# Kernel optimization log

Hardware: AMD Instinct MI355X
Metric: run time of the kernel (lower is better)

## Reference

```python
import jax, jax.numpy as jnp
import numpy as np
from jax import lax


def _gaussian_1d(size=5, std=1.0):
    x = np.arange(size) - (size - 1) / 2.0
    return np.exp(-0.5 * (x / std) ** 2).astype(np.float32)  # scipy.signal.gaussian (unnormalized)


def _conv(x, w):
    # x: (N,1,H,W), w: (O,1,kh,kw), stride 1, SAME padding (matches torch padding=k//2)
    return lax.conv_general_dilated(x, w, (1, 1), 'SAME',
                                    dimension_numbers=('NCHW', 'OIHW', 'NCHW'))


def setup_inputs() -> dict:
    key = jax.random.key(0)
    img = jax.random.normal(key, (8, 1, 1024, 1024), dtype=jnp.float32)

    g = _gaussian_1d(5, 1.0)
    gauss_h = jnp.asarray(g.reshape(1, 1, 1, 5))
    gauss_v = jnp.asarray(g.reshape(1, 1, 5, 1))

    sob = np.array([[1, 0, -1], [2, 0, -2], [1, 0, -1]], dtype=np.float32)
    sobel_h = jnp.asarray(sob.reshape(1, 1, 3, 3))
    sobel_v = jnp.asarray(sob.T.reshape(1, 1, 3, 3))

    f0 = np.array([[0, 0, 0], [0, 1, -1], [0, 0, 0]], dtype=np.float32)
    f45 = np.array([[0, 0, 0], [0, 1, 0], [0, 0, -1]], dtype=np.float32)
    f90 = np.array([[0, 0, 0], [0, 1, 0], [0, -1, 0]], dtype=np.float32)
    f135 = np.array([[0, 0, 0], [0, 1, 0], [-1, 0, 0]], dtype=np.float32)
    f180 = np.array([[0, 0, 0], [-1, 1, 0], [0, 0, 0]], dtype=np.float32)
    f225 = np.array([[-1, 0, 0], [0, 1, 0], [0, 0, 0]], dtype=np.float32)
    f270 = np.array([[0, -1, 0], [0, 1, 0], [0, 0, 0]], dtype=np.float32)
    f315 = np.array([[0, 0, -1], [0, 1, 0], [0, 0, 0]], dtype=np.float32)
    dir_w = jnp.asarray(np.stack([f0, f45, f90, f135, f180, f225, f270, f315])[:, None])  # (8,1,3,3)

    return {"img": img, "gauss_h": gauss_h, "gauss_v": gauss_v,
            "sobel_h": sobel_h, "sobel_v": sobel_v, "dir_w": dir_w}


def reference(img, gauss_h, gauss_v, sobel_h, sobel_v, dir_w):
    THRESHOLD = 2.0
    # separable gaussian blur
    blurred = _conv(_conv(img, gauss_h), gauss_v)  # (N,1,H,W)
    # sobel gradients
    grad_x = _conv(blurred, sobel_h)
    grad_y = _conv(blurred, sobel_v)
    grad_mag = jnp.sqrt(grad_x ** 2 + grad_y ** 2)  # (N,1,H,W)
    # orientation quantized to multiples of 45 deg in [0, 360]
    grad_orientation = jnp.arctan2(grad_y, grad_x) * (180.0 / 3.14159) + 180.0
    grad_orientation = jnp.round(grad_orientation / 45.0) * 45.0
    # directional NMS (vectorized replacement of the batch-looped gather)
    all_filtered = _conv(grad_mag, dir_w)  # (N,8,H,W)
    idx_pos = (jnp.round(grad_orientation / 45.0).astype(jnp.int32)) % 8  # (N,1,H,W)
    idx_neg = (idx_pos + 4) % 8
    sel_pos = jnp.take_along_axis(all_filtered, idx_pos, axis=1)  # (N,1,H,W)
    sel_neg = jnp.take_along_axis(all_filtered, idx_neg, axis=1)
    is_max = jnp.minimum(sel_pos, sel_neg) > 0.0
    thin_edges = jnp.where(is_max, grad_mag, 0.0)
    thresholded = jnp.where(thin_edges < THRESHOLD, 0.0, thin_edges)  # computed but unused, as in source
    del thresholded
    early_threshold = jnp.where(grad_mag < THRESHOLD, 0.0, grad_mag)
    return early_threshold
```

## Files before the change

### kernel.cpp

```cpp
#include <hip/hip_runtime.h>
#include <math.h>


#define TW 64
#define TH 32
#define HALO 3
#define SW (TW + 2 * HALO)
#define SH (TH + 2 * HALO)
#define H_IMG 1024
#define W_IMG 1024

__global__ __launch_bounds__(256) void canny_fused(
    const float* __restrict__ img,
    const float* __restrict__ gauss,
    float* __restrict__ out)
{
    __shared__ float s_img[SH][SW];
    __shared__ float s_t[SH][SW];
    __shared__ float s_b[SH][SW];

    const int tx0 = blockIdx.x * TW;
    const int ty0 = blockIdx.y * TH;
    const int b   = blockIdx.z;
    const int tid = threadIdx.x;

    const float g0 = gauss[0];
    const float g1 = gauss[1];
    const float g2 = gauss[2];

    const float* imgb = img + (size_t)b * (H_IMG * W_IMG);

    for (int i = tid; i < SH * SW; i += 256) {
        int sr = i / SW, sc = i - sr * SW;
        int gy = ty0 + sr - HALO;
        int gx = tx0 + sc - HALO;
        float v = 0.0f;
        if (gy >= 0 && gy < H_IMG && gx >= 0 && gx < W_IMG)
            v = imgb[gy * W_IMG + gx];
        s_img[sr][sc] = v;
    }
    __syncthreads();

    for (int i = tid; i < SH * SW; i += 256) {
        int sr = i / SW, sc = i - sr * SW;
        if (sc >= 2 && sc <= SW - 3) {
            s_t[sr][sc] = g0 * (s_img[sr][sc - 2] + s_img[sr][sc + 2])
                        + g1 * (s_img[sr][sc - 1] + s_img[sr][sc + 1])
                        + g2 *  s_img[sr][sc];
        }
    }
    __syncthreads();

    for (int i = tid; i < SH * SW; i += 256) {
        int sr = i / SW, sc = i - sr * SW;
        if (sr >= 2 && sr <= SH - 3 && sc >= 2 && sc <= SW - 3) {
            int gy = ty0 + sr - HALO;
            int gx = tx0 + sc - HALO;
            float v = 0.0f;
            if (gy >= 0 && gy < H_IMG && gx >= 0 && gx < W_IMG) {
                v = g0 * (s_t[sr - 2][sc] + s_t[sr + 2][sc])
                  + g1 * (s_t[sr - 1][sc] + s_t[sr + 1][sc])
                  + g2 *  s_t[sr][sc];
            }
            s_b[sr][sc] = v;
        }
    }
    __syncthreads();

    float* outb = out + (size_t)b * (H_IMG * W_IMG);
    for (int j = tid; j < TH * TW; j += 256) {
        int ly = j / TW, lx = j - ly * TW;
        int sr = ly + HALO, sc = lx + HALO;
        float tl = s_b[sr - 1][sc - 1], tm = s_b[sr - 1][sc], tr = s_b[sr - 1][sc + 1];
        float ml = s_b[sr    ][sc - 1],                       mr = s_b[sr    ][sc + 1];
        float bl = s_b[sr + 1][sc - 1], bm = s_b[sr + 1][sc], br = s_b[sr + 1][sc + 1];
        float gx = (tl - tr) + 2.0f * (ml - mr) + (bl - br);
        float gy = (tl + 2.0f * tm + tr) - (bl + 2.0f * bm + br);
        float mag = sqrtf(gx * gx + gy * gy);
        outb[(ty0 + ly) * W_IMG + (tx0 + lx)] = (mag < 2.0f) ? 0.0f : mag;
    }
}

extern "C" void kernel_launch(void* const* d_in, const int* in_sizes, int n_in,
                              void* d_out, int out_size, void* d_ws, size_t ws_size,
                              hipStream_t stream) {
    const float* img   = (const float*)d_in[0];
    const float* gauss = (const float*)d_in[1];
    float* out = (float*)d_out;
    const int N = in_sizes[0] / (H_IMG * W_IMG);

    dim3 grid(W_IMG / TW, H_IMG / TH, N);
    canny_fused<<<grid, 256, 0, stream>>>(img, gauss, out);
}
```

Baseline: 117.5 us.

## Vectorize fused Canny kernel with float4 global and shared memory accesses

```diff
diff --git a/kernel.cpp b/kernel.cpp
--- a/kernel.cpp
+++ b/kernel.cpp
@@ -4,20 +4,29 @@
 
 #define TW 64
 #define TH 32
-#define HALO 3
-#define SW (TW + 2 * HALO)
-#define SH (TH + 2 * HALO)
+#define HX 4
+#define HY 3
+#define SW (TW + 2 * HX)
+#define SH (TH + 2 * HY)
+#define NB (SW / 4)
 #define H_IMG 1024
 #define W_IMG 1024
 
-__global__ __launch_bounds__(256) void canny_fused(
+#define SOB(tl, tm, tr, ml, mr, bl, bm, br, dst)                      \
+    {                                                                 \
+        float gx_ = (tl - tr) + 2.0f * (ml - mr) + (bl - br);         \
+        float gy_ = (tl + 2.0f * tm + tr) - (bl + 2.0f * bm + br);    \
+        float mag_ = sqrtf(gx_ * gx_ + gy_ * gy_);                    \
+        dst = (mag_ < 2.0f) ? 0.0f : mag_;                            \
+    }
+
+__global__ __launch_bounds__(256) void canny_fused_v4(
     const float* __restrict__ img,
     const float* __restrict__ gauss,
     float* __restrict__ out)
 {
-    __shared__ float s_img[SH][SW];
-    __shared__ float s_t[SH][SW];
-    __shared__ float s_b[SH][SW];
+    __shared__ float4 s_a[SH][NB];
+    __shared__ float4 s_t[SH][NB];
 
     const int tx0 = blockIdx.x * TW;
     const int ty0 = blockIdx.y * TH;
@@ -29,55 +38,71 @@
     const float g2 = gauss[2];
 
     const float* imgb = img + (size_t)b * (H_IMG * W_IMG);
+    const float4 zero4 = make_float4(0.0f, 0.0f, 0.0f, 0.0f);
 
-    for (int i = tid; i < SH * SW; i += 256) {
-        int sr = i / SW, sc = i - sr * SW;
-        int gy = ty0 + sr - HALO;
-        int gx = tx0 + sc - HALO;
-        float v = 0.0f;
-        if (gy >= 0 && gy < H_IMG && gx >= 0 && gx < W_IMG)
-            v = imgb[gy * W_IMG + gx];
-        s_img[sr][sc] = v;
+    #pragma unroll
+    for (int i = tid; i < SH * NB; i += 256) {
+        int r = i / NB, j = i - r * NB;
+        int gy  = ty0 + r - HY;
+        int gx0 = tx0 + 4 * j - HX;
+        float4 v = zero4;
+        if (gy >= 0 && gy < H_IMG && gx0 >= 0 && gx0 < W_IMG)
+            v = *(const float4*)(imgb + gy * W_IMG + gx0);
+        s_a[r][j] = v;
     }
     __syncthreads();
 
-    for (int i = tid; i < SH * SW; i += 256) {
-        int sr = i / SW, sc = i - sr * SW;
-        if (sc >= 2 && sc <= SW - 3) {
-            s_t[sr][sc] = g0 * (s_img[sr][sc - 2] + s_img[sr][sc + 2])
-                        + g1 * (s_img[sr][sc - 1] + s_img[sr][sc + 1])
-                        + g2 *  s_img[sr][sc];
-        }
+    #pragma unroll
+    for (int i = tid; i < SH * NB; i += 256) {
+        int r = i / NB, j = i - r * NB;
+        float4 A = (j > 0)      ? s_a[r][j - 1] : zero4;
+        float4 B = s_a[r][j];
+        float4 C = (j < NB - 1) ? s_a[r][j + 1] : zero4;
+        float4 t;
+        t.x = g0 * (A.z + B.z) + g1 * (A.w + B.y) + g2 * B.x;
+        t.y = g0 * (A.w + B.w) + g1 * (B.x + B.z) + g2 * B.y;
+        t.z = g0 * (B.x + C.x) + g1 * (B.y + B.w) + g2 * B.z;
+        t.w = g0 * (B.y + C.y) + g1 * (B.z + C.x) + g2 * B.w;
+        s_t[r][j] = t;
     }
     __syncthreads();
 
-    for (int i = tid; i < SH * SW; i += 256) {
-        int sr = i / SW, sc = i - sr * SW;
-        if (sr >= 2 && sr <= SH - 3 && sc >= 2 && sc <= SW - 3) {
-            int gy = ty0 + sr - HALO;
-            int gx = tx0 + sc - HALO;
-            float v = 0.0f;
-            if (gy >= 0 && gy < H_IMG && gx >= 0 && gx < W_IMG) {
-                v = g0 * (s_t[sr - 2][sc] + s_t[sr + 2][sc])
-                  + g1 * (s_t[sr - 1][sc] + s_t[sr + 1][sc])
-                  + g2 *  s_t[sr][sc];
-            }
-            s_b[sr][sc] = v;
-        }
+    #pragma unroll
+    for (int i = tid; i < (SH - 4) * NB; i += 256) {
+        int r2 = i / NB, j = i - r2 * NB;
+        int r = r2 + 2;
+        float4 a = s_t[r - 2][j];
+        float4 bb = s_t[r - 1][j];
+        float4 c = s_t[r][j];
+        float4 d = s_t[r + 1][j];
+        float4 e = s_t[r + 2][j];
+        float4 v;
+        v.x = g0 * (a.x + e.x) + g1 * (bb.x + d.x) + g2 * c.x;
+        v.y = g0 * (a.y + e.y) + g1 * (bb.y + d.y) + g2 * c.y;
+        v.z = g0 * (a.z + e.z) + g1 * (bb.z + d.z) + g2 * c.z;
+        v.w = g0 * (a.w + e.w) + g1 * (bb.w + d.w) + g2 * c.w;
+        int gy  = ty0 + r - HY;
+        int gx0 = tx0 + 4 * j - HX;
+        if (!(gy >= 0 && gy < H_IMG && gx0 >= 0 && gx0 < W_IMG)) v = zero4;
+        s_a[r][j] = v;
     }
     __syncthreads();
 
     float* outb = out + (size_t)b * (H_IMG * W_IMG);
-    for (int j = tid; j < TH * TW; j += 256) {
-        int ly = j / TW, lx = j - ly * TW;
-        int sr = ly + HALO, sc = lx + HALO;
-        float tl = s_b[sr - 1][sc - 1], tm = s_b[sr - 1][sc], tr = s_b[sr - 1][sc + 1];
-        float ml = s_b[sr    ][sc - 1],                       mr = s_b[sr    ][sc + 1];
-        float bl = s_b[sr + 1][sc - 1], bm = s_b[sr + 1][sc], br = s_b[sr + 1][sc + 1];
-        float gx = (tl - tr) + 2.0f * (ml - mr) + (bl - br);
-        float gy = (tl + 2.0f * tm + tr) - (bl + 2.0f * bm + br);
-        float mag = sqrtf(gx * gx + gy * gy);
-        outb[(ty0 + ly) * W_IMG + (tx0 + lx)] = (mag < 2.0f) ? 0.0f : mag;
+    #pragma unroll
+    for (int i = tid; i < TH * (TW / 4); i += 256) {
+        int orow = i >> 4;
+        int oj   = i & 15;
+        int r = orow + HY;
+        float4 Lt = s_a[r - 1][oj], Mt = s_a[r - 1][oj + 1], Rt = s_a[r - 1][oj + 2];
+        float4 Lm = s_a[r    ][oj], Mm = s_a[r    ][oj + 1], Rm = s_a[r    ][oj + 2];
+        float4 Lb = s_a[r + 1][oj], Mb = s_a[r + 1][oj + 1], Rb = s_a[r + 1][oj + 2];
+        float4 o;
+        SOB(Lt.w, Mt.x, Mt.y,  Lm.w, Mm.y,  Lb.w, Mb.x, Mb.y, o.x);
+        SOB(Mt.x, Mt.y, Mt.z,  Mm.x, Mm.z,  Mb.x, Mb.y, Mb.z, o.y);
+        SOB(Mt.y, Mt.z, Mt.w,  Mm.y, Mm.w,  Mb.y, Mb.z, Mb.w, o.z);
+        SOB(Mt.z, Mt.w, Rt.x,  Mm.z, Rm.x,  Mb.z, Mb.w, Rb.x, o.w);
+        *(float4*)(outb + (ty0 + orow) * W_IMG + tx0 + 4 * oj) = o;
     }
 }
 
@@ -90,5 +115,5 @@
     const int N = in_sizes[0] / (H_IMG * W_IMG);
 
     dim3 grid(W_IMG / TW, H_IMG / TH, N);
-    canny_fused<<<grid, 256, 0, stream>>>(img, gauss, out);
+    canny_fused_v4<<<grid, 256, 0, stream>>>(img, gauss, out);
 }
```

New measurement: 111.7 us. -5.0%, faster.

## Replace shared-memory tiling with register row-streaming using float4 loads

Applied to the files above, without the earlier changes.

```diff
diff --git a/kernel.cpp b/kernel.cpp
--- a/kernel.cpp
+++ b/kernel.cpp
@@ -2,82 +2,87 @@
 #include <math.h>
 
 
-#define TW 64
-#define TH 32
-#define HALO 3
-#define SW (TW + 2 * HALO)
-#define SH (TH + 2 * HALO)
 #define H_IMG 1024
 #define W_IMG 1024
+#define W4 (W_IMG / 4)
+#define R 8
 
-__global__ __launch_bounds__(256) void canny_fused(
+__global__ __launch_bounds__(256) void canny_stream(
     const float* __restrict__ img,
     const float* __restrict__ gauss,
     float* __restrict__ out)
 {
-    __shared__ float s_img[SH][SW];
-    __shared__ float s_t[SH][SW];
-    __shared__ float s_b[SH][SW];
+    const int j  = threadIdx.x;
+    const int y0 = blockIdx.x * R;
+    const int b  = blockIdx.y;
 
-    const int tx0 = blockIdx.x * TW;
-    const int ty0 = blockIdx.y * TH;
-    const int b   = blockIdx.z;
-    const int tid = threadIdx.x;
+    const float g0 = gauss[0], g1 = gauss[1], g2 = gauss[2];
+    const float* __restrict__ imgb = img + (size_t)b * (H_IMG * W_IMG);
+    float* __restrict__ outb       = out + (size_t)b * (H_IMG * W_IMG);
+    const int xc = 4 * j;
 
-    const float g0 = gauss[0];
-    const float g1 = gauss[1];
-    const float g2 = gauss[2];
+    float hb[5][6];
+    float bl[3][6];
 
-    const float* imgb = img + (size_t)b * (H_IMG * W_IMG);
+    #pragma unroll
+    for (int it = 0; it < R + 6; ++it) {
+        const int ry = y0 - 3 + it;
+        float* h = hb[it % 5];
+        if (ry >= 0 && ry < H_IMG) {
+            const float* p = imgb + ry * W_IMG + xc;
+            float4 A = make_float4(0.f, 0.f, 0.f, 0.f);
+            float4 C = make_float4(0.f, 0.f, 0.f, 0.f);
+            if (j > 0)      A = *(const float4*)(p - 4);
+            float4 B = *(const float4*)(p);
+            if (j < W4 - 1) C = *(const float4*)(p + 4);
+            h[0] = g0 * (A.y + B.y) + g1 * (A.z + B.x) + g2 * A.w;
+            h[1] = g0 * (A.z + B.z) + g1 * (A.w + B.y) + g2 * B.x;
+            h[2] = g0 * (A.w + B.w) + g1 * (B.x + B.z) + g2 * B.y;
+            h[3] = g0 * (B.x + C.x) + g1 * (B.y + B.w) + g2 * B.z;
+            h[4] = g0 * (B.y + C.y) + g1 * (B.z + C.x) + g2 * B.w;
+            h[5] = g0 * (B.z + C.z) + g1 * (B.w + C.y) + g2 * C.x;
+        } else {
+            #pragma unroll
+            for (int k = 0; k < 6; ++k) h[k] = 0.0f;
+        }
 
-    for (int i = tid; i < SH * SW; i += 256) {
-        int sr = i / SW, sc = i - sr * SW;
-        int gy = ty0 + sr - HALO;
-        int gx = tx0 + sc - HALO;
-        float v = 0.0f;
-        if (gy >= 0 && gy < H_IMG && gx >= 0 && gx < W_IMG)
-            v = imgb[gy * W_IMG + gx];
-        s_img[sr][sc] = v;
-    }
-    __syncthreads();
+        if (it >= 4) {
+            const int by = ry - 2;
+            float* o = bl[(it - 4) % 3];
+            if (by >= 0 && by < H_IMG) {
+                const float* h0 = hb[(it - 4) % 5];
+                const float* h1 = hb[(it - 3) % 5];
+                const float* h2 = hb[(it - 2) % 5];
+                const float* h3 = hb[(it - 1) % 5];
+                const float* h4 = hb[(it    ) % 5];
+                #pragma unroll
+                for (int k = 0; k < 6; ++k)
+                    o[k] = g0 * (h0[k] + h4[k]) + g1 * (h1[k] + h3[k]) + g2 * h2[k];
+                if (j == 0)      o[0] = 0.0f;
+                if (j == W4 - 1) o[5] = 0.0f;
+            } else {
+                #pragma unroll
+                for (int k = 0; k < 6; ++k) o[k] = 0.0f;
+            }
+        }
 
-    for (int i = tid; i < SH * SW; i += 256) {
-        int sr = i / SW, sc = i - sr * SW;
-        if (sc >= 2 && sc <= SW - 3) {
-            s_t[sr][sc] = g0 * (s_img[sr][sc - 2] + s_img[sr][sc + 2])
-                        + g1 * (s_img[sr][sc - 1] + s_img[sr][sc + 1])
-                        + g2 *  s_img[sr][sc];
+        if (it >= 6) {
+            const int oy = ry - 3;
+            const float* T  = bl[(it - 6) % 3];
+            const float* M  = bl[(it - 5) % 3];
+            const float* Bo = bl[(it - 4) % 3];
+            float4 o4;
+            float* po = (float*)&o4;
+            #pragma unroll
+            for (int k = 0; k < 4; ++k) {
+                float gx = (T[k] - T[k + 2]) + 2.0f * (M[k] - M[k + 2]) + (Bo[k] - Bo[k + 2]);
+                float gy = (T[k] + 2.0f * T[k + 1] + T[k + 2])
+                         - (Bo[k] + 2.0f * Bo[k + 1] + Bo[k + 2]);
+                float mag = sqrtf(gx * gx + gy * gy);
+                po[k] = (mag < 2.0f) ? 0.0f : mag;
+            }
+            *(float4*)(outb + oy * W_IMG + xc) = o4;
         }
-    }
-    __syncthreads();
-
-    for (int i = tid; i < SH * SW; i += 256) {
-        int sr = i / SW, sc = i - sr * SW;
-        if (sr >= 2 && sr <= SH - 3 && sc >= 2 && sc <= SW - 3) {
-            int gy = ty0 + sr - HALO;
-            int gx = tx0 + sc - HALO;
-            float v = 0.0f;
-            if (gy >= 0 && gy < H_IMG && gx >= 0 && gx < W_IMG) {
-                v = g0 * (s_t[sr - 2][sc] + s_t[sr + 2][sc])
-                  + g1 * (s_t[sr - 1][sc] + s_t[sr + 1][sc])
-                  + g2 *  s_t[sr][sc];
-            }
-            s_b[sr][sc] = v;
-        }
-    }
-    __syncthreads();
-
-    float* outb = out + (size_t)b * (H_IMG * W_IMG);
-    for (int j = tid; j < TH * TW; j += 256) {
-        int ly = j / TW, lx = j - ly * TW;
-        int sr = ly + HALO, sc = lx + HALO;
-        float tl = s_b[sr - 1][sc - 1], tm = s_b[sr - 1][sc], tr = s_b[sr - 1][sc + 1];
-        float ml = s_b[sr    ][sc - 1],                       mr = s_b[sr    ][sc + 1];
-        float bl = s_b[sr + 1][sc - 1], bm = s_b[sr + 1][sc], br = s_b[sr + 1][sc + 1];
-        float gx = (tl - tr) + 2.0f * (ml - mr) + (bl - br);
-        float gy = (tl + 2.0f * tm + tr) - (bl + 2.0f * bm + br);
-        float mag = sqrtf(gx * gx + gy * gy);
-        outb[(ty0 + ly) * W_IMG + (tx0 + lx)] = (mag < 2.0f) ? 0.0f : mag;
     }
 }
 
@@ -89,6 +94,6 @@
     float* out = (float*)d_out;
     const int N = in_sizes[0] / (H_IMG * W_IMG);
 
-    dim3 grid(W_IMG / TW, H_IMG / TH, N);
-    canny_fused<<<grid, 256, 0, stream>>>(img, gauss, out);
+    dim3 grid(H_IMG / R, N);
+    canny_stream<<<grid, 256, 0, stream>>>(img, gauss, out);
 }
```

Measured after the change: 100.9 us. -14.1%, faster.
